# Performance work log

Hardware: AMD Instinct MI355X
Metric: run time of the kernel (lower is better)

## Reference

```python
import jax, jax.numpy as jnp
import numpy as np

HEADS = 8
DIM_HEAD = 64
NUM_PATHWAYS = 281
SCALE = DIM_HEAD ** -0.5


def setup_inputs() -> dict:
    key = jax.random.key(0)
    k1, k2 = jax.random.split(key)
    b, n, dim = 4, 12281, 512  # n = 281 pathway tokens + 12000 histology patch tokens
    x = jax.random.normal(k1, (b, n, dim), dtype=jnp.float32)
    W_qkv = jax.random.normal(k2, (dim, 3 * HEADS * DIM_HEAD), dtype=jnp.float32) * 0.02
    return {"x": x, "W_qkv": W_qkv}


def reference(x, W_qkv):
    b, n, _ = x.shape
    h, d, m = HEADS, DIM_HEAD, NUM_PATHWAYS
    qkv = x @ W_qkv  # [b, n, 3*h*d]
    q, k, v = jnp.split(qkv, 3, axis=-1)
    # [b, n, h*d] -> [b, h, n, d]
    to_bhnd = lambda t: t.reshape(b, n, h, d).transpose(0, 2, 1, 3)
    q, k, v = to_bhnd(q), to_bhnd(k), to_bhnd(v)
    q = q * SCALE

    q_path, q_hist = q[:, :, :m], q[:, :, m:]
    k_path, k_hist = k[:, :, :m], k[:, :, m:]
    v_path, v_hist = v[:, :, :m], v[:, :, m:]

    # histology queries attend to pathway keys: [b, h, n_hist, m]
    attn_hist = jax.nn.softmax(jnp.einsum('bhid,bhjd->bhij', q_hist, k_path), axis=-1)
    # pathway queries attend to histology keys: [b, h, m, n_hist]
    attn_path = jax.nn.softmax(jnp.einsum('bhid,bhjd->bhij', q_path, k_hist), axis=-1)

    out_pathways = jnp.einsum('bhij,bhjd->bhid', attn_hist, v_path)   # [b, h, n_hist, d]
    out_histology = jnp.einsum('bhij,bhjd->bhid', attn_path, v_hist)  # [b, h, m, d]

    cross_token = jnp.concatenate([out_pathways, out_histology], axis=2)  # [b, h, n, d]
    return cross_token.transpose(0, 2, 1, 3).reshape(b, n, h * d)
```

## Files before the change

kernel.cpp:

```cpp
#include <hip/hip_runtime.h>
#include <hip/hip_bf16.h>

#define BATCH  4
#define NTOK   12281
#define DIMIN  512
#define HEADS  8
#define DHEAD  64
#define MPATH  281
#define NHIST  12000
#define QKVC   1536
#define QSCALE 0.180336884f
#define ROWS   (BATCH * NTOK)
#define MPAD   49152
#define NSPLIT 16
#define KSPL   768
#define PROWS  320
#define HROWS  12032
#define M1B    1024
#define M0B    1504
#define QPAD   4096

typedef __attribute__((ext_vector_type(8)))  short        short8v;
typedef __attribute__((ext_vector_type(4)))  float        f32x4;
typedef __attribute__((ext_vector_type(16))) float        f32x16;
typedef __attribute__((ext_vector_type(4)))  unsigned int uint4v;

__device__ __forceinline__ unsigned short f2bf(float f) {
    unsigned x = __builtin_bit_cast(unsigned, f);
    return (unsigned short)((x + 0x7fffu + ((x >> 16) & 1u)) >> 16);
}
__device__ __forceinline__ unsigned pk2(float a, float b) {
    return (unsigned)f2bf(a) | ((unsigned)f2bf(b) << 16);
}
__device__ __forceinline__ unsigned pk2n(float a, float b) {
    unsigned r;
    asm("v_cvt_pk_bf16_f32 %0, %1, %2" : "=v"(r) : "v"(a), "v"(b));
    return r;
}
__device__ __forceinline__ void plswap(unsigned &a, unsigned &b) {
    asm("v_permlane32_swap_b32 %0, %1" : "+v"(a), "+v"(b));
}
__device__ __forceinline__ float fexp2(float x) {
    return __builtin_amdgcn_exp2f(x);
}
__device__ __forceinline__ short8v ld8(const unsigned short* p) {
    return *reinterpret_cast<const short8v*>(p);
}
__device__ __forceinline__ f32x16 MFMA32(short8v a, short8v b, f32x16 c) {
    return __builtin_amdgcn_mfma_f32_32x32x16_bf16(a, b, c, 0, 0, 0);
}
__device__ __forceinline__ void gl16(const char* g, char* l) {
    __builtin_amdgcn_global_load_lds(
        (const __attribute__((address_space(1))) unsigned int*)g,
        (__attribute__((address_space(3))) unsigned int*)l, 16, 0, 0);
}

__global__ __launch_bounds__(256)
void convert_x(const float* __restrict__ x, unsigned short* __restrict__ xb)
{
    size_t i = ((size_t)blockIdx.x * 256 + threadIdx.x) * 8;
    if (i >= (size_t)MPAD * DIMIN) return;
    uint4v o;
    if (i < (size_t)ROWS * DIMIN) {
        float4 a = *reinterpret_cast<const float4*>(x + i);
        float4 b = *reinterpret_cast<const float4*>(x + i + 4);
        o[0] = pk2(a.x, a.y); o[1] = pk2(a.z, a.w);
        o[2] = pk2(b.x, b.y); o[3] = pk2(b.z, b.w);
    } else {
        o[0] = o[1] = o[2] = o[3] = 0u;
    }
    *reinterpret_cast<uint4v*>(xb + i) = o;
}

__global__ __launch_bounds__(256)
void wt_convert(const float* __restrict__ w, unsigned short* __restrict__ wt)
{
    __shared__ unsigned short Ls[64][72];
    const int k0 = blockIdx.x * 64;
    const int n0 = blockIdx.y * 64;
    const int t  = threadIdx.x;
    const int lr = t >> 2;
    const int c0 = (t & 3) * 16;

    const float* sp = w + (size_t)(k0 + lr) * QKVC + n0 + c0;
    #pragma unroll
    for (int j = 0; j < 16; j += 4) {
        float4 a = *reinterpret_cast<const float4*>(sp + j);
        Ls[lr][c0 + j + 0] = f2bf(a.x);
        Ls[lr][c0 + j + 1] = f2bf(a.y);
        Ls[lr][c0 + j + 2] = f2bf(a.z);
        Ls[lr][c0 + j + 3] = f2bf(a.w);
    }
    __syncthreads();

    alignas(16) unsigned short tmp[16];
    #pragma unroll
    for (int j = 0; j < 16; ++j) tmp[j] = Ls[c0 + j][lr];
    unsigned short* dp = wt + (size_t)(n0 + lr) * DIMIN + k0 + c0;
    *reinterpret_cast<short8v*>(dp)     = *reinterpret_cast<short8v*>(&tmp[0]);
    *reinterpret_cast<short8v*>(dp + 8) = *reinterpret_cast<short8v*>(&tmp[8]);
}

__global__ __launch_bounds__(256)
void pad_fill(unsigned short* kpth, unsigned short* vpth,
              unsigned short* khst, unsigned short* vhst)
{
    int i = blockIdx.x * 256 + threadIdx.x;
    const int PPAD = (PROWS - MPATH) * DHEAD;
    const int HPAD = (HROWS - NHIST) * DHEAD;
    if (i < 32 * PPAD) {
        int bh = i / PPAD, r = i - bh * PPAD;
        size_t off = ((size_t)bh * PROWS + MPATH) * DHEAD + r;
        kpth[off] = 0; vpth[off] = 0;
    }
    if (i < 32 * HPAD) {
        int bh = i / HPAD, r = i - bh * HPAD;
        size_t off = ((size_t)bh * HROWS + NHIST) * DHEAD + r;
        khst[off] = 0; vhst[off] = 0;
    }
}

__global__ __launch_bounds__(256, 2)
void qkv_mfma(const unsigned short* __restrict__ xb, const unsigned short* __restrict__ wt,
              unsigned short* __restrict__ qb,
              unsigned short* __restrict__ kpth, unsigned short* __restrict__ khst,
              unsigned short* __restrict__ vpth, unsigned short* __restrict__ vhst)
{
    __shared__ char lds[65536];
    const int tid  = threadIdx.x;
    const int lane = tid & 63;
    const int wid  = tid >> 6;
    const int wr   = wid >> 1;
    const int wc   = wid & 1;

    int id  = blockIdx.x;
    int wg  = (id & 7) * 576 + (id >> 3);
    const int mt = wg / 12, nt = wg - mt * 12;
    const int bm = mt * 128, bn = nt * 128;

    const int arow0 = tid >> 3;
    const int acolS = ((tid & 7) << 4) ^ ((arow0 & 7) << 4);
    const char* xsrc = (const char*)xb + (((size_t)(bm + arow0)) << 10) + acolS;
    const char* wsrc = (const char*)wt + (((size_t)(bn + arow0)) << 10) + acolS;
    char* ldsA = lds + wid * 1024;
    char* ldsB = lds + 16384 + wid * 1024;

    const int rA   = wr * 64 + (lane & 15);
    const int rB   = wc * 64 + (lane & 15);
    const int hi16 = (lane >> 4) << 4;
    const int sxA  = (rA & 7) << 4;
    const int sxB  = (rB & 7) << 4;

    f32x4 acc[4][4];
    #pragma unroll
    for (int m = 0; m < 4; ++m)
        #pragma unroll
        for (int n = 0; n < 4; ++n)
            #pragma unroll
            for (int r = 0; r < 4; ++r) acc[m][n][r] = 0.f;

    auto STAGE = [&](int bufofs, int ks) {
        const char* xs = xsrc + (size_t)ks * 128;
        const char* ws = wsrc + (size_t)ks * 128;
        #pragma unroll
        for (int i = 0; i < 4; ++i)
            gl16(xs + ((size_t)i << 15), ldsA + bufofs + i * 4096);
        #pragma unroll
        for (int i = 0; i < 4; ++i)
            gl16(ws + ((size_t)i << 15), ldsB + bufofs + i * 4096);
    };

    STAGE(0, 0);
    asm volatile("s_waitcnt vmcnt(0)" ::: "memory");
    __syncthreads();

    for (int ks = 0; ks < 8; ++ks) {
        const int cur = ks & 1;
        if (ks < 7) STAGE((cur ^ 1) * 32768, ks + 1);

        const char* A = lds + cur * 32768;
        const char* B = A + 16384;
        #pragma unroll
        for (int kk = 0; kk < 2; ++kk) {
            short8v a[4], b[4];
            #pragma unroll
            for (int m = 0; m < 4; ++m)
                a[m] = *reinterpret_cast<const short8v*>(
                    A + (rA + m * 16) * 128 + ((kk * 64 + hi16) ^ sxA));
            #pragma unroll
            for (int n = 0; n < 4; ++n)
                b[n] = *reinterpret_cast<const short8v*>(
                    B + (rB + n * 16) * 128 + ((kk * 64 + hi16) ^ sxB));
            #pragma unroll
            for (int m = 0; m < 4; ++m)
                #pragma unroll
                for (int n = 0; n < 4; ++n)
                    acc[m][n] = __builtin_amdgcn_mfma_f32_16x16x32_bf16(
                        a[m], b[n], acc[m][n], 0, 0, 0);
        }
        asm volatile("s_waitcnt vmcnt(0)" ::: "memory");
        __syncthreads();
    }

    unsigned short* cl = reinterpret_cast<unsigned short*>(lds);
    const int crow0 = (lane >> 4) * 4;
    const int ccol  = lane & 15;
    #pragma unroll
    for (int n = 0; n < 4; ++n) {
        const int gcb = bn + wc * 64 + n * 16;
        const float scl = (gcb < 512) ? QSCALE : 1.f;
        #pragma unroll
        for (int m = 0; m < 4; ++m) {
            #pragma unroll
            for (int r = 0; r < 4; ++r) {
                int row = wr * 64 + m * 16 + crow0 + r;
                int col = wc * 64 + n * 16 + ccol;
                cl[row * 136 + col] = f2bf(acc[m][n][r] * scl);
            }
        }
    }
    __syncthreads();

    #pragma unroll
    for (int i = 0; i < 8; ++i) {
        const int chunk = tid + i * 256;
        const int row = chunk >> 4;
        const int c8  = (chunk & 15) * 8;
        const int grow = bm + row;
        if (grow < ROWS) {
            uint4v val = *reinterpret_cast<const uint4v*>(cl + row * 136 + c8);
            const int gcol  = bn + c8;
            const int which = gcol >> 9;
            const int rem   = gcol & 511;
            const int hh = rem >> 6, dd = rem & 63;
            const int bb = grow / NTOK;
            const int nn = grow - bb * NTOK;
            const int bh = bb * HEADS + hh;
            unsigned short* dst;
            if (which == 0) {
                dst = qb + ((size_t)bh * NTOK + nn) * DHEAD + dd;
            } else if (which == 1) {
                dst = (nn < MPATH) ? kpth + ((size_t)bh * PROWS + nn) * DHEAD + dd
                                   : khst + ((size_t)bh * HROWS + (nn - MPATH)) * DHEAD + dd;
            } else {
                dst = (nn < MPATH) ? vpth + ((size_t)bh * PROWS + nn) * DHEAD + dd
                                   : vhst + ((size_t)bh * HROWS + (nn - MPATH)) * DHEAD + dd;
            }
            *reinterpret_cast<uint4v*>(dst) = val;
        }
    }
}

__global__ __launch_bounds__(256)
void transpose64(const unsigned short* __restrict__ src, unsigned short* __restrict__ dst,
                 int nrpad)
{
    __shared__ unsigned short Ls[64][72];
    const int bh = blockIdx.y;
    const int r0 = blockIdx.x * 64;
    const unsigned short* s = src + (size_t)bh * nrpad * DHEAD;
    unsigned short*       d = dst + (size_t)bh * nrpad * DHEAD;

    const int t  = threadIdx.x;
    const int lr = t >> 2;
    const int c0 = (t & 3) * 16;

    const unsigned short* sp = s + (size_t)(r0 + lr) * DHEAD + c0;
    *reinterpret_cast<short8v*>(&Ls[lr][c0])     = *reinterpret_cast<const short8v*>(sp);
    *reinterpret_cast<short8v*>(&Ls[lr][c0 + 8]) = *reinterpret_cast<const short8v*>(sp + 8);
    __syncthreads();

    alignas(16) unsigned short tmp[16];
    #pragma unroll
    for (int j = 0; j < 16; ++j) tmp[j] = Ls[c0 + j][lr];
    const int T  = (r0 + c0) >> 5;
    const int kk = (r0 + c0) & 31;
    unsigned short* dp = d + (((size_t)T * 64 + lr) << 5) + kk;
    *reinterpret_cast<short8v*>(dp)     = *reinterpret_cast<short8v*>(&tmp[0]);
    *reinterpret_cast<short8v*>(dp + 8) = *reinterpret_cast<short8v*>(&tmp[8]);
}

__global__ __launch_bounds__(256, 2)
void fused_attn(const unsigned short* __restrict__ qbuf,
                const unsigned short* __restrict__ kpth, const unsigned short* __restrict__ khst,
                const unsigned short* __restrict__ vtp,  const unsigned short* __restrict__ vth,
                float* __restrict__ out,
                float* __restrict__ pl, float* __restrict__ po)
{
    const int wave = threadIdx.x >> 6;
    const int lane = threadIdx.x & 63;
    const int hi   = lane >> 5;
    const int ql   = lane & 31;

    int bh, pw, sp = 0;
    bool mode0;
    if (blockIdx.x < M1B) {
        mode0 = false;
        const int xcd = blockIdx.x & 7;
        const int jj  = blockIdx.x >> 3;
        bh = jj >> 2;
        const int rem = jj & 3;
        sp = xcd + 8 * (rem & 1);
        pw = (rem >> 1) * 4 + wave;
        if (pw >= 5) return;
    } else {
        mode0 = true;
        const int b0  = blockIdx.x - M1B;
        const int xcd = b0 & 7;
        const int i   = b0 >> 3;
        const int g   = i / 47;
        bh = xcd + 8 * g;
        pw = (i - g * 47) * 4 + wave;
    }

    const int q0 = mode0 ? (MPATH + pw * 64) : (pw * 64);
    const unsigned short* qra = qbuf + ((size_t)bh * NTOK + (q0 + ql)) * DHEAD + hi * 8;
    const unsigned short* qrb = qra + (size_t)32 * DHEAD;
    short8v qA0 = ld8(qra),      qA1 = ld8(qra + 16);
    short8v qA2 = ld8(qra + 32), qA3 = ld8(qra + 48);
    short8v qB0 = ld8(qrb),      qB1 = ld8(qrb + 16);
    short8v qB2 = ld8(qrb + 32), qB3 = ld8(qrb + 48);

    const unsigned short* kr;
    const unsigned short* vb;
    int ntiles;
    if (mode0) {
        kr = kpth + (size_t)bh * PROWS * DHEAD + ql * DHEAD + hi * 8;
        vb = vtp  + (size_t)bh * PROWS * DHEAD + ql * 32 + hi * 8;
        ntiles = 9;
    } else {
        kr = khst + ((size_t)bh * HROWS + (size_t)sp * KSPL) * DHEAD + ql * DHEAD + hi * 8;
        vb = vth  + (size_t)bh * HROWS * DHEAD + (size_t)sp * 24 * 2048 + ql * 32 + hi * 8;
        ntiles = (sp == NSPLIT - 1) ? 15 : 24;
    }

    f32x16 o0, o1, o2, o3, SZ;
    #pragma unroll
    for (int r = 0; r < 16; ++r) { o0[r] = 0.f; o1[r] = 0.f; o2[r] = 0.f; o3[r] = 0.f; SZ[r] = 0.f; }
    float lA = 0.f, lB = 0.f;

    short8v kf0 = ld8(kr), kf1 = ld8(kr + 16), kf2 = ld8(kr + 32), kf3 = ld8(kr + 48);

    for (int t = 0; t < ntiles; ++t) {
        const unsigned short* vp = vb + (size_t)t * 2048;
        short8v vf0 = ld8(vp);
        short8v vf1 = ld8(vp + 16);
        short8v vf2 = ld8(vp + 1024);
        short8v vf3 = ld8(vp + 1040);

        __builtin_amdgcn_s_setprio(1);
        f32x16 sA = MFMA32(kf0, qA0, SZ);
        sA = MFMA32(kf1, qA1, sA);
        sA = MFMA32(kf2, qA2, sA);
        sA = MFMA32(kf3, qA3, sA);
        f32x16 sB = MFMA32(kf0, qB0, SZ);
        sB = MFMA32(kf1, qB1, sB);
        sB = MFMA32(kf2, qB2, sB);
        sB = MFMA32(kf3, qB3, sB);
        __builtin_amdgcn_s_setprio(0);

        if (t + 1 < ntiles) {
            const unsigned short* kn = kr + (size_t)(t + 1) * 2048;
            kf0 = ld8(kn);      kf1 = ld8(kn + 16);
            kf2 = ld8(kn + 32); kf3 = ld8(kn + 48);
        }

        float psA = 0.f, psB = 0.f;
        if (mode0 && t == 8) {
            #pragma unroll
            for (int r = 0; r < 16; ++r) {
                int krow = (r & 3) + 8 * (r >> 2) + 4 * hi;
                float eA = (256 + krow >= MPATH) ? 0.f : fexp2(sA[r]);
                float eB = (256 + krow >= MPATH) ? 0.f : fexp2(sB[r]);
                sA[r] = eA; psA += eA;
                sB[r] = eB; psB += eB;
            }
        } else {
            #pragma unroll
            for (int r = 0; r < 16; ++r) {
                float eA = fexp2(sA[r]); sA[r] = eA; psA += eA;
                float eB = fexp2(sB[r]); sB[r] = eB; psB += eB;
            }
        }
        lA += psA; lB += psB;

        unsigned A0 = pk2n(sA[0],  sA[1]),  A1 = pk2n(sA[2],  sA[3]);
        unsigned A2 = pk2n(sA[4],  sA[5]),  A3 = pk2n(sA[6],  sA[7]);
        unsigned A4 = pk2n(sA[8],  sA[9]),  A5 = pk2n(sA[10], sA[11]);
        unsigned A6 = pk2n(sA[12], sA[13]), A7 = pk2n(sA[14], sA[15]);
        plswap(A0, A2); plswap(A1, A3); plswap(A4, A6); plswap(A5, A7);
        uint4v wA0, wA1;
        wA0[0] = A0; wA0[1] = A1; wA0[2] = A2; wA0[3] = A3;
        wA1[0] = A4; wA1[1] = A5; wA1[2] = A6; wA1[3] = A7;
        short8v paA0 = __builtin_bit_cast(short8v, wA0);
        short8v paA1 = __builtin_bit_cast(short8v, wA1);
        unsigned B0 = pk2n(sB[0],  sB[1]),  B1 = pk2n(sB[2],  sB[3]);
        unsigned B2 = pk2n(sB[4],  sB[5]),  B3 = pk2n(sB[6],  sB[7]);
        unsigned B4 = pk2n(sB[8],  sB[9]),  B5 = pk2n(sB[10], sB[11]);
        unsigned B6 = pk2n(sB[12], sB[13]), B7 = pk2n(sB[14], sB[15]);
        plswap(B0, B2); plswap(B1, B3); plswap(B4, B6); plswap(B5, B7);
        uint4v wB0, wB1;
        wB0[0] = B0; wB0[1] = B1; wB0[2] = B2; wB0[3] = B3;
        wB1[0] = B4; wB1[1] = B5; wB1[2] = B6; wB1[3] = B7;
        short8v paB0 = __builtin_bit_cast(short8v, wB0);
        short8v paB1 = __builtin_bit_cast(short8v, wB1);

        __builtin_amdgcn_s_setprio(1);
        o0 = MFMA32(paA0, vf0, o0);
        o0 = MFMA32(paA1, vf1, o0);
        o1 = MFMA32(paA0, vf2, o1);
        o1 = MFMA32(paA1, vf3, o1);
        o2 = MFMA32(paB0, vf0, o2);
        o2 = MFMA32(paB1, vf1, o2);
        o3 = MFMA32(paB0, vf2, o3);
        o3 = MFMA32(paB1, vf3, o3);
        __builtin_amdgcn_s_setprio(0);
    }

    const float lAr = lA + __shfl_xor(lA, 32);
    const float lBr = lB + __shfl_xor(lB, 32);

    if (mode0) {
        const int bb = bh >> 3, hh = bh & 7;
        const float liA = 1.0f / lAr;
        const float liB = 1.0f / lBr;
        #pragma unroll
        for (int r = 0; r < 16; ++r) {
            const int row = (r & 3) + 8 * (r >> 2) + 4 * hi;
            {
                float invr = __shfl(liA, row);
                float* op = out + ((size_t)bb * NTOK + (pw * 64 + row)) * (HEADS * DHEAD) + hh * DHEAD;
                op[ql]      = o0[r] * invr;
                op[32 + ql] = o1[r] * invr;
            }
            const int tokB = pw * 64 + 32 + row;
            if (tokB < NHIST) {
                float invr = __shfl(liB, row);
                float* op = out + ((size_t)bb * NTOK + tokB) * (HEADS * DHEAD) + hh * DHEAD;
                op[ql]      = o2[r] * invr;
                op[32 + ql] = o3[r] * invr;
            }
        }
    } else {
        const size_t pbase = ((size_t)bh * NSPLIT + sp) * MPATH;
        if (hi == 0) {
            if (q0 + ql < MPATH)      pl[pbase + q0 + ql]      = lAr;
            if (q0 + 32 + ql < MPATH) pl[pbase + q0 + 32 + ql] = lBr;
        }
        #pragma unroll
        for (int r = 0; r < 16; ++r) {
            const int row = (r & 3) + 8 * (r >> 2) + 4 * hi;
            const int qqA = q0 + row;
            if (qqA < MPATH) {
                float* pp = po + (pbase + qqA) * DHEAD;
                pp[ql]      = o0[r];
                pp[32 + ql] = o1[r];
            }
            const int qqB = q0 + 32 + row;
            if (qqB < MPATH) {
                float* pp = po + (pbase + qqB) * DHEAD;
                pp[ql]      = o2[r];
                pp[32 + ql] = o3[r];
            }
        }
    }
}

__global__ __launch_bounds__(256)
void combine_kernel(const float* __restrict__ pl, const float* __restrict__ po,
                    float* __restrict__ out)
{
    const int idx = blockIdx.x * 256 + threadIdx.x;
    const int dd  = idx & 63;
    const int r   = idx >> 6;
    if (r >= BATCH * HEADS * MPATH) return;
    const int bh = r / MPATH;
    const int jq = r - bh * MPATH;

    const size_t pbase = ((size_t)bh * NSPLIT) * MPATH + jq;
    float L = 0.f, acc = 0.f;
    #pragma unroll
    for (int s = 0; s < NSPLIT; ++s) {
        L   += pl[pbase + (size_t)s * MPATH];
        acc += po[(pbase + (size_t)s * MPATH) * DHEAD + dd];
    }
    const int bb = bh >> 3, hh = bh & 7;
    out[((size_t)bb * NTOK + (NHIST + jq)) * (HEADS * DHEAD) + hh * DHEAD + dd] = acc / L;
}

extern "C" void kernel_launch(void* const* d_in, const int* in_sizes, int n_in,
                              void* d_out, int out_size, void* d_ws, size_t ws_size,
                              hipStream_t stream)
{
    (void)in_sizes; (void)n_in; (void)out_size; (void)ws_size;
    const float* x = (const float*)d_in[0];
    const float* w = (const float*)d_in[1];
    float* out = (float*)d_out;

    const size_t QEL = (size_t)32 * NTOK * DHEAD + QPAD;
    const size_t PEL = (size_t)32 * PROWS * DHEAD;
    const size_t HEL = (size_t)32 * HROWS * DHEAD;

    unsigned short* qb   = (unsigned short*)d_ws;
    unsigned short* kpth = qb   + QEL;
    unsigned short* khst = kpth + PEL;
    unsigned short* vpth = khst + HEL;
    unsigned short* vhst = vpth + PEL;
    unsigned short* vtp  = vhst + HEL;
    unsigned short* vth  = vtp  + PEL;
    unsigned short* xb   = vth  + HEL;
    unsigned short* wtb  = xb   + (size_t)MPAD * DIMIN;
    float* pl = (float*)(wtb + (size_t)QKVC * DIMIN);
    float* po = pl + (size_t)32 * NSPLIT * MPATH;

    convert_x<<<(MPAD * DIMIN / 8 + 255) / 256, 256, 0, stream>>>(x, xb);
    wt_convert<<<dim3(DIMIN / 64, QKVC / 64), 256, 0, stream>>>(w, wtb);
    pad_fill<<<312, 256, 0, stream>>>(kpth, vpth, khst, vhst);

    qkv_mfma<<<(MPAD / 128) * (QKVC / 128), 256, 0, stream>>>(xb, wtb, qb,
                                                              kpth, khst, vpth, vhst);

    transpose64<<<dim3(PROWS / 64, 32), 256, 0, stream>>>(vpth, vtp, PROWS);
    transpose64<<<dim3(HROWS / 64, 32), 256, 0, stream>>>(vhst, vth, HROWS);

    fused_attn<<<M1B + M0B, 256, 0, stream>>>(qb, kpth, khst, vtp, vth, out, pl, po);

    const int rows = BATCH * HEADS * MPATH;
    combine_kernel<<<(rows * DHEAD + 255) / 256, 256, 0, stream>>>(pl, po, out);
}
```

Before: 296.6 us.

## Prefetch V tiles one step ahead and pack mode1 waves densely

Result: faster. 282.2 us (-4.8%).

```diff
diff --git a/kernel.cpp b/kernel.cpp
--- a/kernel.cpp
+++ b/kernel.cpp
@@ -16,7 +16,7 @@
 #define KSPL   768
 #define PROWS  320
 #define HROWS  12032
-#define M1B    1024
+#define M1B    640
 #define M0B    1504
 #define QPAD   4096
 
@@ -280,6 +280,76 @@
     *reinterpret_cast<short8v*>(dp + 8) = *reinterpret_cast<short8v*>(&tmp[8]);
 }
 
+#define ATTN_BODY(VC0,VC1,VC2,VC3,VN0,VN1,VN2,VN3,TT)                      \
+  do {                                                                     \
+    __builtin_amdgcn_s_setprio(1);                                         \
+    f32x16 sA = MFMA32(kf0, qA0, SZ);                                      \
+    sA = MFMA32(kf1, qA1, sA);                                             \
+    sA = MFMA32(kf2, qA2, sA);                                             \
+    sA = MFMA32(kf3, qA3, sA);                                             \
+    f32x16 sB = MFMA32(kf0, qB0, SZ);                                      \
+    sB = MFMA32(kf1, qB1, sB);                                             \
+    sB = MFMA32(kf2, qB2, sB);                                             \
+    sB = MFMA32(kf3, qB3, sB);                                             \
+    __builtin_amdgcn_s_setprio(0);                                         \
+    if ((TT) + 1 < ntiles) {               \
+      const unsigned short* kn = kr + (size_t)((TT) + 1) * 2048;           \
+      kf0 = ld8(kn);      kf1 = ld8(kn + 16);                              \
+      kf2 = ld8(kn + 32); kf3 = ld8(kn + 48);                              \
+      const unsigned short* vn = vb + (size_t)((TT) + 1) * 2048;           \
+      VN0 = ld8(vn);        VN1 = ld8(vn + 16);                            \
+      VN2 = ld8(vn + 1024); VN3 = ld8(vn + 1040);                          \
+    }                                                                      \
+    float psA = 0.f, psB = 0.f;                                            \
+    if (mode0 && (TT) == 8) {                   \
+      _Pragma("unroll")                                                    \
+      for (int r = 0; r < 16; ++r) {                                       \
+        int krow = (r & 3) + 8 * (r >> 2) + 4 * hi;                        \
+        float eA = (256 + krow >= MPATH) ? 0.f : fexp2(sA[r]);             \
+        float eB = (256 + krow >= MPATH) ? 0.f : fexp2(sB[r]);             \
+        sA[r] = eA; psA += eA;                                             \
+        sB[r] = eB; psB += eB;                                             \
+      }                                                                    \
+    } else {                                                               \
+      _Pragma("unroll")                                                    \
+      for (int r = 0; r < 16; ++r) {                                       \
+        float eA = fexp2(sA[r]); sA[r] = eA; psA += eA;                    \
+        float eB = fexp2(sB[r]); sB[r] = eB; psB += eB;                    \
+      }                                                                    \
+    }                                                                      \
+    lA += psA; lB += psB;                                                  \
+    unsigned A0 = pk2n(sA[0],  sA[1]),  A1 = pk2n(sA[2],  sA[3]);          \
+    unsigned A2 = pk2n(sA[4],  sA[5]),  A3 = pk2n(sA[6],  sA[7]);          \
+    unsigned A4 = pk2n(sA[8],  sA[9]),  A5 = pk2n(sA[10], sA[11]);         \
+    unsigned A6 = pk2n(sA[12], sA[13]), A7 = pk2n(sA[14], sA[15]);         \
+    plswap(A0, A2); plswap(A1, A3); plswap(A4, A6); plswap(A5, A7);        \
+    uint4v wA0, wA1;                                                       \
+    wA0[0] = A0; wA0[1] = A1; wA0[2] = A2; wA0[3] = A3;                    \
+    wA1[0] = A4; wA1[1] = A5; wA1[2] = A6; wA1[3] = A7;                    \
+    short8v paA0 = __builtin_bit_cast(short8v, wA0);                       \
+    short8v paA1 = __builtin_bit_cast(short8v, wA1);                       \
+    unsigned B0 = pk2n(sB[0],  sB[1]),  B1 = pk2n(sB[2],  sB[3]);          \
+    unsigned B2 = pk2n(sB[4],  sB[5]),  B3 = pk2n(sB[6],  sB[7]);          \
+    unsigned B4 = pk2n(sB[8],  sB[9]),  B5 = pk2n(sB[10], sB[11]);         \
+    unsigned B6 = pk2n(sB[12], sB[13]), B7 = pk2n(sB[14], sB[15]);         \
+    plswap(B0, B2); plswap(B1, B3); plswap(B4, B6); plswap(B5, B7);        \
+    uint4v wB0, wB1;                                                       \
+    wB0[0] = B0; wB0[1] = B1; wB0[2] = B2; wB0[3] = B3;                    \
+    wB1[0] = B4; wB1[1] = B5; wB1[2] = B6; wB1[3] = B7;                    \
+    short8v paB0 = __builtin_bit_cast(short8v, wB0);                       \
+    short8v paB1 = __builtin_bit_cast(short8v, wB1);                       \
+    __builtin_amdgcn_s_setprio(1);                                         \
+    o0 = MFMA32(paA0, VC0, o0);                                            \
+    o0 = MFMA32(paA1, VC1, o0);                                            \
+    o1 = MFMA32(paA0, VC2, o1);                                            \
+    o1 = MFMA32(paA1, VC3, o1);                                            \
+    o2 = MFMA32(paB0, VC0, o2);                                            \
+    o2 = MFMA32(paB1, VC1, o2);                                            \
+    o3 = MFMA32(paB0, VC2, o3);                                            \
+    o3 = MFMA32(paB1, VC3, o3);                                            \
+    __builtin_amdgcn_s_setprio(0);                                         \
+  } while (0)
+
 __global__ __launch_bounds__(256, 2)
 void fused_attn(const unsigned short* __restrict__ qbuf,
                 const unsigned short* __restrict__ kpth, const unsigned short* __restrict__ khst,
@@ -297,12 +367,13 @@
     if (blockIdx.x < M1B) {
         mode0 = false;
         const int xcd = blockIdx.x & 7;
-        const int jj  = blockIdx.x >> 3;
-        bh = jj >> 2;
-        const int rem = jj & 3;
-        sp = xcd + 8 * (rem & 1);
-        pw = (rem >> 1) * 4 + wave;
-        if (pw >= 5) return;
+        const int j   = blockIdx.x >> 3;
+        const int w   = j * 4 + wave;
+        const int spi = w / 160;
+        const int rem = w - spi * 160;
+        bh = rem / 5;
+        pw = rem - bh * 5;
+        sp = xcd + 8 * spi;
     } else {
         mode0 = true;
         const int b0  = blockIdx.x - M1B;
@@ -340,81 +411,15 @@
     float lA = 0.f, lB = 0.f;
 
     short8v kf0 = ld8(kr), kf1 = ld8(kr + 16), kf2 = ld8(kr + 32), kf3 = ld8(kr + 48);
-
-    for (int t = 0; t < ntiles; ++t) {
-        const unsigned short* vp = vb + (size_t)t * 2048;
-        short8v vf0 = ld8(vp);
-        short8v vf1 = ld8(vp + 16);
-        short8v vf2 = ld8(vp + 1024);
-        short8v vf3 = ld8(vp + 1040);
-
-        __builtin_amdgcn_s_setprio(1);
-        f32x16 sA = MFMA32(kf0, qA0, SZ);
-        sA = MFMA32(kf1, qA1, sA);
-        sA = MFMA32(kf2, qA2, sA);
-        sA = MFMA32(kf3, qA3, sA);
-        f32x16 sB = MFMA32(kf0, qB0, SZ);
-        sB = MFMA32(kf1, qB1, sB);
-        sB = MFMA32(kf2, qB2, sB);
-        sB = MFMA32(kf3, qB3, sB);
-        __builtin_amdgcn_s_setprio(0);
-
-        if (t + 1 < ntiles) {
-            const unsigned short* kn = kr + (size_t)(t + 1) * 2048;
-            kf0 = ld8(kn);      kf1 = ld8(kn + 16);
-            kf2 = ld8(kn + 32); kf3 = ld8(kn + 48);
-        }
-
-        float psA = 0.f, psB = 0.f;
-        if (mode0 && t == 8) {
-            #pragma unroll
-            for (int r = 0; r < 16; ++r) {
-                int krow = (r & 3) + 8 * (r >> 2) + 4 * hi;
-                float eA = (256 + krow >= MPATH) ? 0.f : fexp2(sA[r]);
-                float eB = (256 + krow >= MPATH) ? 0.f : fexp2(sB[r]);
-                sA[r] = eA; psA += eA;
-                sB[r] = eB; psB += eB;
-            }
-        } else {
-            #pragma unroll
-            for (int r = 0; r < 16; ++r) {
-                float eA = fexp2(sA[r]); sA[r] = eA; psA += eA;
-                float eB = fexp2(sB[r]); sB[r] = eB; psB += eB;
-            }
-        }
-        lA += psA; lB += psB;
-
-        unsigned A0 = pk2n(sA[0],  sA[1]),  A1 = pk2n(sA[2],  sA[3]);
-        unsigned A2 = pk2n(sA[4],  sA[5]),  A3 = pk2n(sA[6],  sA[7]);
-        unsigned A4 = pk2n(sA[8],  sA[9]),  A5 = pk2n(sA[10], sA[11]);
-        unsigned A6 = pk2n(sA[12], sA[13]), A7 = pk2n(sA[14], sA[15]);
-        plswap(A0, A2); plswap(A1, A3); plswap(A4, A6); plswap(A5, A7);
-        uint4v wA0, wA1;
-        wA0[0] = A0; wA0[1] = A1; wA0[2] = A2; wA0[3] = A3;
-        wA1[0] = A4; wA1[1] = A5; wA1[2] = A6; wA1[3] = A7;
-        short8v paA0 = __builtin_bit_cast(short8v, wA0);
-        short8v paA1 = __builtin_bit_cast(short8v, wA1);
-        unsigned B0 = pk2n(sB[0],  sB[1]),  B1 = pk2n(sB[2],  sB[3]);
-        unsigned B2 = pk2n(sB[4],  sB[5]),  B3 = pk2n(sB[6],  sB[7]);
-        unsigned B4 = pk2n(sB[8],  sB[9]),  B5 = pk2n(sB[10], sB[11]);
-        unsigned B6 = pk2n(sB[12], sB[13]), B7 = pk2n(sB[14], sB[15]);
-        plswap(B0, B2); plswap(B1, B3); plswap(B4, B6); plswap(B5, B7);
-        uint4v wB0, wB1;
-        wB0[0] = B0; wB0[1] = B1; wB0[2] = B2; wB0[3] = B3;
-        wB1[0] = B4; wB1[1] = B5; wB1[2] = B6; wB1[3] = B7;
-        short8v paB0 = __builtin_bit_cast(short8v, wB0);
-        short8v paB1 = __builtin_bit_cast(short8v, wB1);
-
-        __builtin_amdgcn_s_setprio(1);
-        o0 = MFMA32(paA0, vf0, o0);
-        o0 = MFMA32(paA1, vf1, o0);
-        o1 = MFMA32(paA0, vf2, o1);
-        o1 = MFMA32(paA1, vf3, o1);
-        o2 = MFMA32(paB0, vf0, o2);
-        o2 = MFMA32(paB1, vf1, o2);
-        o3 = MFMA32(paB0, vf2, o3);
-        o3 = MFMA32(paB1, vf3, o3);
-        __builtin_amdgcn_s_setprio(0);
+    short8v va0 = ld8(vb),        va1 = ld8(vb + 16);
+    short8v va2 = ld8(vb + 1024), va3 = ld8(vb + 1040);
+    short8v vb0 = va0, vb1 = va1, vb2 = va2, vb3 = va3;
+
+    for (int t = 0;;) {
+        ATTN_BODY(va0, va1, va2, va3, vb0, vb1, vb2, vb3, t);
+        if (++t >= ntiles) break;
+        ATTN_BODY(vb0, vb1, vb2, vb3, va0, va1, va2, va3, t);
+        if (++t >= ntiles) break;
     }
 
     const float lAr = lA + __shfl_xor(lA, 32);
```
